# Performance work log

Measured on AMD Instinct MI355X. Metric: run time of the kernel, lower is better.

Reference implementation:

```python
import jax, jax.numpy as jnp
import numpy as np

WIDTH = 64
RANK = 4
CLEVEL = 1
MLEVEL = 2
NB = 4
HID1, HID2 = 64, 128  # DenseNet hidden sizes for phi/psi kernel networks


def setup_inputs() -> dict:
    key = jax.random.key(0)
    ks = jax.random.split(key, 24)
    b, s = 2, 256

    def g(k, shape, fan):
        return jax.random.normal(k, shape, jnp.float32) / np.sqrt(fan)

    L = MLEVEL + 1
    inp = {
        "x": jax.random.normal(ks[0], (b, s, s, 1), jnp.float32),
        "a": jax.random.uniform(ks[1], (b, s, s, 2), jnp.float32),
        # lifting p: Linear(3, width)
        "pW": g(ks[2], (3, WIDTH), 3), "pb": jnp.zeros((WIDTH,), jnp.float32),
        # projection q: DenseNet([width, 2*width, 1], ReLU)
        "q1W": g(ks[3], (WIDTH, 2 * WIDTH), WIDTH), "q1b": jnp.zeros((2 * WIDTH,), jnp.float32),
        "q2W": g(ks[4], (2 * WIDTH, 1), 2 * WIDTH), "q2b": jnp.zeros((1,), jnp.float32),
        # low-rank kernel nets phi/psi: DenseNet([3, 64, 128, width*rank]), one per block (stacked)
        "phiW1": g(ks[5], (NB, 3, HID1), 3), "phib1": jnp.zeros((NB, HID1), jnp.float32),
        "phiW2": g(ks[6], (NB, HID1, HID2), HID1), "phib2": jnp.zeros((NB, HID2), jnp.float32),
        "phiW3": g(ks[7], (NB, HID2, WIDTH * RANK), HID2), "phib3": jnp.zeros((NB, WIDTH * RANK), jnp.float32),
        "psiW1": g(ks[8], (NB, 3, HID1), 3), "psib1": jnp.zeros((NB, HID1), jnp.float32),
        "psiW2": g(ks[9], (NB, HID1, HID2), HID1), "psib2": jnp.zeros((NB, HID2), jnp.float32),
        "psiW3": g(ks[10], (NB, HID2, WIDTH * RANK), HID2), "psib3": jnp.zeros((NB, WIDTH * RANK), jnp.float32),
        # per-block LayerNorm(width)
        "lnG": jnp.ones((NB, WIDTH), jnp.float32), "lnB": jnp.zeros((NB, WIDTH), jnp.float32),
        # per-block multi-level local-correction 3x3 convs (OIHW), levels 0..MLEVEL
        "convW": g(ks[11], (NB, L, WIDTH, WIDTH, 3, 3), WIDTH * 9),
        "convb": jnp.zeros((NB, L, WIDTH), jnp.float32),
    }
    return inp


def _mlp3(x, W1, b1, W2, b2, W3, b3):
    h = jax.nn.relu(x @ W1 + b1)
    h = jax.nn.relu(h @ W2 + b2)
    return h @ W3 + b3


def _lowrank(v, a, phi_p, psi_p):
    # v: (b, sx, sy, w) features; a: (b, sx, sy, 3) coords+input
    b, sx, sy, w = v.shape
    n = sx * sy
    af = a.reshape(b, n, 3)
    vf = v.reshape(b, n, w)
    phi = _mlp3(af, *phi_p).reshape(b, n, w, RANK)  # (b,n,w,r)
    psi = _mlp3(af, *psi_p).reshape(b, n, w, RANK)
    # K(u)(x_m) = sum_r phi_r(x_m) * (1/n) sum_n psi_r(y_n) u(y_n), per channel
    y = jnp.einsum("bnwr,bnw->bwr", psi, vf) / n
    out = jnp.einsum("bnwr,bwr->bnw", phi, y)
    return out.reshape(b, sx, sy, w)


def _conv3x3(x, W, bias):
    # x: (b,c,h,w) NCHW, W: (o,i,3,3)
    y = jax.lax.conv_general_dilated(x, W, (1, 1), "SAME",
                                     dimension_numbers=("NCHW", "OIHW", "NCHW"))
    return y + bias[None, :, None, None]


def _local_correction(xc, Ws, bs):
    # xc: (b,c,h,w); Ws: (L,o,i,3,3); multi-level conv pyramid, bilinear upsample back
    h, w = xc.shape[2], xc.shape[3]
    out = _conv3x3(xc, Ws[0], bs[0])
    for l in range(1, Ws.shape[0]):
        xl = xc[:, :, :: 2 ** l, :: 2 ** l]
        yl = _conv3x3(xl, Ws[l], bs[l])
        out = out + jax.image.resize(yl, yl.shape[:2] + (h, w), method="bilinear")
    return out


def _layernorm(x, g, b, eps=1e-5):
    mu = jnp.mean(x, axis=-1, keepdims=True)
    var = jnp.mean(jnp.square(x - mu), axis=-1, keepdims=True)
    return (x - mu) * jax.lax.rsqrt(var + eps) * g + b


def reference(x, a, pW, pb, q1W, q1b, q2W, q2b,
              phiW1, phib1, phiW2, phib2, phiW3, phib3,
              psiW1, psib1, psiW2, psib2, psiW3, psib3,
              lnG, lnB, convW, convb):
    b, sx, sy, _ = x.shape
    xa = jnp.concatenate([a, x], axis=-1)  # (b,sx,sy,3)
    acat = xa
    h = xa @ pW + pb  # lift to width
    c = 2 ** CLEVEL
    for i in range(NB):
        # local correction branch (NCHW conv pyramid)
        x1 = _local_correction(h.transpose(0, 3, 1, 2), convW[i], convb[i]).transpose(0, 2, 3, 1)
        # low-rank kernel integral on coarsened grid, then bilinear upsample
        hd = h[:, ::c, ::c]
        ad = acat[:, ::c, ::c]
        x2 = _lowrank(hd, ad,
                      (phiW1[i], phib1[i], phiW2[i], phib2[i], phiW3[i], phib3[i]),
                      (psiW1[i], psib1[i], psiW2[i], psib2[i], psiW3[i], psib3[i]))
        x2 = jax.image.resize(x2.transpose(0, 3, 1, 2), (b, WIDTH, sx, sy),
                              method="bilinear").transpose(0, 2, 3, 1)
        h = _layernorm(x1 + x2, lnG[i], lnB[i])
        if i != NB - 1:
            h = jax.nn.relu(h)
    h1 = jax.nn.relu(h @ q1W + q1b)
    return h1 @ q2W + q2b
```

## Files before the change

kernel.cpp:

```cpp
#include <hip/hip_runtime.h>
#include <cstddef>
#include <cstdint>


static constexpr size_t OFF_X1     = 0;
static constexpr size_t OFF_YL1    = 4194304;
static constexpr size_t OFF_YL2    = 5242880;
static constexpr size_t OFF_HBF    = 5505024;
static constexpr size_t OFF_H2PSI  = 9699328;
static constexpr size_t OFF_H2PHI  = 11796480;
static constexpr size_t OFF_CWTBF  = 13893632;
static constexpr size_t OFF_Q1BF   = 14114816;
static constexpr size_t OFF_W2T    = 14118912;
static constexpr size_t OFF_GPART  = 14151680;
static constexpr size_t OFF_SVP    = 18345984;
static constexpr size_t OFF_G      = 18378752;
static constexpr size_t OFF_SV     = 18395136;
static constexpr size_t OFF_C      = 18395264;
static constexpr size_t OFF_D      = 18411648;

typedef __attribute__((ext_vector_type(8)))  short bf16x8_t;
typedef __attribute__((ext_vector_type(16))) float f32x16_t;

__device__ inline float wave_sum64(float v) {
    v += __shfl_xor(v, 1);
    v += __shfl_xor(v, 2);
    v += __shfl_xor(v, 4);
    v += __shfl_xor(v, 8);
    v += __shfl_xor(v, 16);
    v += __shfl_xor(v, 32);
    return v;
}

__device__ inline unsigned short f2bf(float f) {
    uint32_t u = __float_as_uint(f);
    uint32_t r = u + 0x7FFFu + ((u >> 16) & 1u);
    return (unsigned short)(r >> 16);
}
__device__ inline float bf2f(unsigned short u) {
    return __uint_as_float((uint32_t)u << 16);
}
__device__ inline void bf8_to_f(uint4 u, float* d) {
    unsigned uv[4] = {u.x, u.y, u.z, u.w};
#pragma unroll
    for (int i = 0; i < 4; ++i) {
        d[2 * i]     = __uint_as_float((uv[i] & 0xFFFFu) << 16);
        d[2 * i + 1] = __uint_as_float(uv[i] & 0xFFFF0000u);
    }
}

__device__ inline size_t fullpix(int b, int n) {
    return (size_t)(b * 65536 + (n >> 7) * 512 + ((n & 127) << 1));
}

struct Lerp { int i0, i1; float f; };
__device__ inline Lerp lcoord(int o, float r, float off, int Sin) {
    float s = fmaxf(fmaf((float)o, r, off), 0.f);
    Lerp L;
    L.i0 = (int)s;
    L.f  = s - (float)L.i0;
    L.i1 = min(L.i0 + 1, Sin - 1);
    return L;
}

__global__ __launch_bounds__(256) void k_setup(const float* __restrict__ convW,
                                               unsigned short* __restrict__ cwt,
                                               const float* __restrict__ q1W,
                                               unsigned short* __restrict__ q1bf,
                                               const float* __restrict__ psiW2,
                                               const float* __restrict__ phiW2,
                                               unsigned short* __restrict__ w2t,
                                               const float* __restrict__ x,
                                               const float* __restrict__ a,
                                               const float* __restrict__ pW,
                                               const float* __restrict__ pb,
                                               unsigned short* __restrict__ hbf) {
    int bid = blockIdx.x;
    int t = threadIdx.x;
    if (bid < 1728) {
        int idx = bid * 256 + t;
        if (idx >= 442368) return;
        int j    = idx & 7;
        int oc   = (idx >> 3) & 63;
        int hi   = (idx >> 9) & 1;
        int kq   = (idx >> 10) & 3;
        int rest = idx >> 12;
        int tap  = rest % 9;
        int il   = rest / 9;
        int ic   = kq * 16 + hi * 8 + j;
        cwt[idx] = f2bf(convW[((size_t)(il * 64 + oc) * 64 + ic) * 9 + tap]);
    } else if (bid < 1760) {
        int idx = (bid - 1728) * 256 + t;
        int k = idx & 63;
        int j = idx >> 6;
        q1bf[j * 64 + k] = f2bf(q1W[k * 128 + j]);
    } else if (bid < 2016) {
        int idx = (bid - 1760) * 256 + t;
        int jj = idx & 7;
        int lo = (idx >> 3) & 31;
        int hi = (idx >> 8) & 1;
        int kq = (idx >> 9) & 3;
        int jt = (idx >> 11) & 3;
        int i  = (idx >> 13) & 3;
        int m  = idx >> 15;
        int k  = kq * 16 + hi * 8 + jj;
        int j  = jt * 32 + lo;
        const float* W2 = m ? phiW2 : psiW2;
        w2t[idx] = f2bf(W2[(size_t)i * 8192 + k * 128 + j]);
    } else {
        int p = (bid - 2016) * 256 + t;
        float a0 = a[(size_t)p * 2 + 0];
        float a1 = a[(size_t)p * 2 + 1];
        float xv = x[p];
        float vals[64];
#pragma unroll
        for (int c = 0; c < 64; ++c)
            vals[c] = fmaf(a0, pW[c], fmaf(a1, pW[64 + c], fmaf(xv, pW[128 + c], pb[c])));
        unsigned short us[64];
#pragma unroll
        for (int c = 0; c < 64; ++c) us[c] = f2bf(vals[c]);
        unsigned short* bp = hbf + (size_t)p * 64;
#pragma unroll
        for (int c = 0; c < 64; c += 8)
            *(uint4*)(bp + c) = *(uint4*)(us + c);
    }
}

__global__ __launch_bounds__(256) void k_convmlp(
    const unsigned short* __restrict__ hbf,
    const unsigned short* __restrict__ wbf,
    const float* __restrict__ convb,
    unsigned short* __restrict__ x1, unsigned short* __restrict__ yl1,
    unsigned short* __restrict__ yl2,
    const float* __restrict__ a, const float* __restrict__ x,
    const float* __restrict__ W1a, const float* __restrict__ b1a,
    const float* __restrict__ b2a,
    const float* __restrict__ W1b, const float* __restrict__ b1b,
    const float* __restrict__ b2b,
    const unsigned short* __restrict__ w2t,
    unsigned short* __restrict__ H2a, unsigned short* __restrict__ H2b,
    int iter) {
    __shared__ unsigned short Ald[20736];
    int bid = blockIdx.x;
    int t = threadIdx.x;

    if (bid >= 672) {
        int blk = bid - 672;
        int m = blk >> 9;
        int px0 = (blk & 511) << 6;
        const float* W1 = m ? W1b : W1a;
        const float* b1 = m ? b1b : b1a;
        const float* b2 = m ? b2b : b2a;
        unsigned short* H2 = m ? H2b : H2a;

        int w    = t >> 6;
        int lane = t & 63;
        int lo   = lane & 31;
        int hi   = lane >> 5;

        int pxlA = px0 + lo, pxlB = px0 + 32 + lo;
        int bA = pxlA >> 14;
        size_t apA = fullpix(bA, pxlA & 16383);
        size_t apB = fullpix(bA, pxlB & 16383);
        float a0A = a[apA * 2], a1A = a[apA * 2 + 1], xvA = x[apA];
        float a0B = a[apB * 2], a1B = a[apB * 2 + 1], xvB = x[apB];

        bf16x8_t faA[4], faB[4];
#pragma unroll
        for (int kq = 0; kq < 4; ++kq) {
            unsigned short tA[8], tB[8];
#pragma unroll
            for (int jj = 0; jj < 8; ++jj) {
                int k = kq * 16 + hi * 8 + jj;
                float w1a = W1[k], w1b = W1[64 + k], w1c = W1[128 + k], bb = b1[k];
                tA[jj] = f2bf(fmaxf(fmaf(a0A, w1a, fmaf(a1A, w1b, fmaf(xvA, w1c, bb))), 0.f));
                tB[jj] = f2bf(fmaxf(fmaf(a0B, w1a, fmaf(a1B, w1b, fmaf(xvB, w1c, bb))), 0.f));
            }
            faA[kq] = *(bf16x8_t*)tA;
            faB[kq] = *(bf16x8_t*)tB;
        }
        const unsigned short* wb =
            w2t + (size_t)(((m * 4 + iter) * 4 + w) * 4) * 512 + hi * 256 + lo * 8;
        f32x16_t accA = {}, accB = {};
#pragma unroll
        for (int kq = 0; kq < 4; ++kq) {
            bf16x8_t fb = *(const bf16x8_t*)(wb + kq * 512);
            accA = __builtin_amdgcn_mfma_f32_32x32x16_bf16(faA[kq], fb, accA, 0, 0, 0);
            accB = __builtin_amdgcn_mfma_f32_32x32x16_bf16(faB[kq], fb, accB, 0, 0, 0);
        }
        float bias2 = b2[w * 32 + lo];
#pragma unroll
        for (int reg = 0; reg < 16; ++reg) {
            int row = (reg & 3) + 8 * (reg >> 2) + 4 * hi;
            H2[(size_t)(px0 + row) * 128 + w * 32 + lo]      = f2bf(fmaxf(accA[reg] + bias2, 0.f));
            H2[(size_t)(px0 + 32 + row) * 128 + w * 32 + lo] = f2bf(fmaxf(accB[reg] + bias2, 0.f));
        }
        return;
    }

    int lvl, tix, Sl, st, tpr;
    if (bid < 512)      { lvl = 0; tix = bid;       Sl = 256; st = 1; tpr = 16; }
    else if (bid < 640) { lvl = 1; tix = bid - 512; Sl = 128; st = 2; tpr = 8;  }
    else                { lvl = 2; tix = bid - 640; Sl = 64;  st = 4; tpr = 4;  }
    int tpb = tpr * tpr;
    int b = tix / tpb;
    int r = tix - b * tpb;
    int y0 = (r / tpr) * 16, x0 = (r % tpr) * 16;

    for (int c = t; c < 2592; c += 256) {
        int lin = c >> 3, slot = c & 7;
        int ty = lin / 18, tx = lin - ty * 18;
        int oy = y0 + ty - 1, ox = x0 + tx - 1;
        uint4 val = make_uint4(0u, 0u, 0u, 0u);
        if ((unsigned)oy < (unsigned)Sl && (unsigned)ox < (unsigned)Sl) {
            const unsigned short* src =
                hbf + (((size_t)(b * 256 + oy * st) * 256 + ox * st) << 6) + (slot << 3);
            val = *(const uint4*)src;
        }
        int byte = (lin << 7) + (((slot ^ (lin & 7))) << 4);
        *(uint4*)((char*)Ald + byte) = val;
    }
    __syncthreads();

    int w    = t >> 6;
    int lane = t & 63;
    int lo   = lane & 31;
    int hi   = lane >> 5;
    f32x16_t acc00 = {}, acc01 = {}, acc10 = {}, acc11 = {};

    const unsigned short* wbase =
        wbf + (size_t)(iter * 3 + lvl) * 36864 + hi * 512 + lo * 8;

    int yA0 = 4 * w + (lo >> 4);
    int xA  = lo & 15;

    bf16x8_t v0c[4], v1c[4], v0n[4], v1n[4];
#pragma unroll
    for (int kq = 0; kq < 4; ++kq) {
        v0c[kq] = *(const bf16x8_t*)(wbase + kq * 1024);
        v1c[kq] = *(const bf16x8_t*)(wbase + kq * 1024 + 256);
    }
#pragma unroll
    for (int tap = 0; tap < 9; ++tap) {
        if (tap < 8) {
#pragma unroll
            for (int kq = 0; kq < 4; ++kq) {
                int keo = ((tap + 1) * 4 + kq) * 1024;
                v0n[kq] = *(const bf16x8_t*)(wbase + keo);
                v1n[kq] = *(const bf16x8_t*)(wbase + keo + 256);
            }
        }
        int dy = tap / 3, dx = tap - dy * 3;
        int lin0 = (yA0 + dy) * 18 + (xA + dx);
        int lin1 = lin0 + 36;
#pragma unroll
        for (int kq = 0; kq < 4; ++kq) {
            int icb = (kq << 5) + (hi << 4);
            int a0b = ((lin0 << 7) + icb) ^ ((lin0 & 7) << 4);
            int a1b = ((lin1 << 7) + icb) ^ ((lin1 & 7) << 4);
            bf16x8_t va0 = *(bf16x8_t*)((char*)Ald + a0b);
            bf16x8_t va1 = *(bf16x8_t*)((char*)Ald + a1b);
            acc00 = __builtin_amdgcn_mfma_f32_32x32x16_bf16(va0, v0c[kq], acc00, 0, 0, 0);
            acc01 = __builtin_amdgcn_mfma_f32_32x32x16_bf16(va0, v1c[kq], acc01, 0, 0, 0);
            acc10 = __builtin_amdgcn_mfma_f32_32x32x16_bf16(va1, v0c[kq], acc10, 0, 0, 0);
            acc11 = __builtin_amdgcn_mfma_f32_32x32x16_bf16(va1, v1c[kq], acc11, 0, 0, 0);
        }
#pragma unroll
        for (int kq = 0; kq < 4; ++kq) { v0c[kq] = v0n[kq]; v1c[kq] = v1n[kq]; }
    }

    unsigned short* out = (lvl == 0) ? x1 : (lvl == 1 ? yl1 : yl2);
    const float* bias = convb + (iter * 3 + lvl) * 64;
    float bias0 = bias[lo];
    float bias1 = bias[32 + lo];
#pragma unroll
    for (int reg = 0; reg < 16; ++reg) {
        int row = (reg & 3) + 8 * (reg >> 2) + 4 * hi;
        int yt  = 4 * w + (row >> 4);
        int xt  = row & 15;
        size_t pix0 = ((size_t)(b * Sl + y0 + yt) * Sl + (x0 + xt)) << 6;
        out[pix0 + lo]      = f2bf(acc00[reg] + bias0);
        out[pix0 + 32 + lo] = f2bf(acc01[reg] + bias1);
        size_t pix1 = ((size_t)(b * Sl + y0 + yt + 2) * Sl + (x0 + xt)) << 6;
        out[pix1 + lo]      = f2bf(acc10[reg] + bias0);
        out[pix1 + 32 + lo] = f2bf(acc11[reg] + bias1);
    }
}

__global__ __launch_bounds__(256) void k_gpart(const unsigned short* __restrict__ hbf,
                                               const unsigned short* __restrict__ H2psi,
                                               float* __restrict__ Gpart,
                                               float* __restrict__ svpart) {
    __shared__ float vt[4096];
    __shared__ float h2t[8192];
    int blk = blockIdx.x;
    int b = blk >> 8;
    int n0 = (blk & 255) << 6;
    int t = threadIdx.x;
    int pxq = t >> 2, qq = t & 3;
    int sw = (pxq & 7) << 4;
    {
        const unsigned short* src = hbf + fullpix(b, n0 + pxq) * 64 + qq * 16;
        uint4 u0 = *(const uint4*)src;
        uint4 u1 = *(const uint4*)(src + 8);
        float f[16];
        bf8_to_f(u0, f);
        bf8_to_f(u1, f + 8);
#pragma unroll
        for (int j = 0; j < 4; ++j) {
            int byte = (pxq * 256 + qq * 64 + j * 16) ^ sw;
            *(float4*)((char*)vt + byte) = make_float4(f[4 * j], f[4 * j + 1],
                                                       f[4 * j + 2], f[4 * j + 3]);
        }
        const unsigned short* hsrc = H2psi + ((size_t)(b * 16384 + n0 + pxq)) * 128 + qq * 32;
#pragma unroll
        for (int rr = 0; rr < 4; ++rr) {
            uint4 hu = *(const uint4*)(hsrc + rr * 8);
            float g[8];
            bf8_to_f(hu, g);
            int byte0 = (pxq * 512 + qq * 128 + rr * 32) ^ sw;
            int byte1 = (pxq * 512 + qq * 128 + rr * 32 + 16) ^ sw;
            *(float4*)((char*)h2t + byte0) = make_float4(g[0], g[1], g[2], g[3]);
            *(float4*)((char*)h2t + byte1) = make_float4(g[4], g[5], g[6], g[7]);
        }
    }
    __syncthreads();

    int wt_ = (t >> 5) << 3;
    int kt  = (t & 31) << 2;
    float acc[8][4];
#pragma unroll
    for (int i = 0; i < 8; ++i)
#pragma unroll
        for (int j = 0; j < 4; ++j) acc[i][j] = 0.f;

#pragma unroll 4
    for (int nn = 0; nn < 64; ++nn) {
        int nsw = (nn & 7) << 4;
        float4 hv = *(float4*)((char*)h2t + ((nn * 512 + kt * 4) ^ nsw));
        float4 v0 = *(float4*)((char*)vt + ((nn * 256 + wt_ * 4) ^ nsw));
        float4 v1 = *(float4*)((char*)vt + ((nn * 256 + wt_ * 4 + 16) ^ nsw));
        float vv[8] = {v0.x, v0.y, v0.z, v0.w, v1.x, v1.y, v1.z, v1.w};
        float hh[4] = {hv.x, hv.y, hv.z, hv.w};
#pragma unroll
        for (int i = 0; i < 8; ++i)
#pragma unroll
            for (int j = 0; j < 4; ++j) acc[i][j] = fmaf(vv[i], hh[j], acc[i][j]);
    }

    float* gp = Gpart + (size_t)blk * 8192;
#pragma unroll
    for (int i = 0; i < 8; ++i)
        *(float4*)&gp[(wt_ + i) * 128 + kt] =
            make_float4(acc[i][0], acc[i][1], acc[i][2], acc[i][3]);

    if (t < 64) {
        float s = 0.f;
#pragma unroll 8
        for (int p = 0; p < 64; ++p)
            s += *(float*)((char*)vt + ((p * 256 + t * 4) ^ ((p & 7) << 4)));
        svpart[blk * 64 + t] = s;
    }
}

__global__ __launch_bounds__(256) void k_gred(const float* __restrict__ Gpart,
                                              const float* __restrict__ svpart,
                                              float* __restrict__ G,
                                              float* __restrict__ sv) {
    __shared__ float red[4][64];
    int blk = blockIdx.x;
    int t = threadIdx.x;
    if (blk < 256) {
        int b  = blk >> 7;
        int es = (blk & 127) << 6;
        int e  = es + (t & 63);
        int cg = t >> 6;
        float s = 0.f;
        const float* gp = Gpart + ((size_t)(b * 256 + cg * 64)) * 8192 + e;
#pragma unroll 8
        for (int c = 0; c < 64; ++c) s += gp[(size_t)c * 8192];
        red[cg][t & 63] = s;
        __syncthreads();
        if (t < 64)
            G[b * 8192 + es + t] = red[0][t] + red[1][t] + red[2][t] + red[3][t];
    } else {
        int b = blk - 256;
        int w = t & 63, cg = t >> 6;
        float s = 0.f;
        const float* sp = svpart + ((size_t)(b * 256 + cg * 64)) * 64 + w;
#pragma unroll 8
        for (int c = 0; c < 64; ++c) s += sp[c * 64];
        red[cg][w] = s;
        __syncthreads();
        if (t < 64) sv[b * 64 + t] = red[0][t] + red[1][t] + red[2][t] + red[3][t];
    }
}

__global__ __launch_bounds__(256) void k_yc(const float* __restrict__ G,
                                            const float* __restrict__ sv,
                                            const float* __restrict__ W3psi,
                                            const float* __restrict__ b3psi,
                                            const float* __restrict__ W3phi,
                                            const float* __restrict__ b3phi,
                                            float* __restrict__ C,
                                            float* __restrict__ D) {
    __shared__ float ybar[256];
    int bq = blockIdx.x;
    int b = bq >> 4, q = bq & 15;
    int t = threadIdx.x;
    {
        int o = t, w = o >> 2;
        const float* gp = &G[(size_t)(b * 64 + w) * 128];
        float s0 = 0.f, s1 = 0.f, s2 = 0.f, s3 = 0.f;
#pragma unroll 4
        for (int k = 0; k < 128; k += 4) {
            s0 = fmaf(W3psi[(k + 0) * 256 + o], gp[k + 0], s0);
            s1 = fmaf(W3psi[(k + 1) * 256 + o], gp[k + 1], s1);
            s2 = fmaf(W3psi[(k + 2) * 256 + o], gp[k + 2], s2);
            s3 = fmaf(W3psi[(k + 3) * 256 + o], gp[k + 3], s3);
        }
        float s = b3psi[o] * sv[b * 64 + w] + ((s0 + s1) + (s2 + s3));
        ybar[o] = s * (1.f / 16384.f);
    }
    __syncthreads();
#pragma unroll
    for (int rep = 0; rep < 2; ++rep) {
        int e = q * 512 + rep * 256 + t;
        int w = e >> 7, k = e & 127;
        const float* wp = &W3phi[k * 256 + w * 4];
        C[b * 8192 + e] = fmaf(wp[0], ybar[w * 4],
                          fmaf(wp[1], ybar[w * 4 + 1],
                          fmaf(wp[2], ybar[w * 4 + 2], wp[3] * ybar[w * 4 + 3])));
    }
    if (q == 0 && t < 64) {
        int w = t;
        D[b * 64 + w] = b3phi[w * 4] * ybar[w * 4] + b3phi[w * 4 + 1] * ybar[w * 4 + 1]
                      + b3phi[w * 4 + 2] * ybar[w * 4 + 2] + b3phi[w * 4 + 3] * ybar[w * 4 + 3];
    }
}

__global__ __launch_bounds__(256) void k_x2c(const unsigned short* __restrict__ H2phi,
                                             const float* __restrict__ C,
                                             const float* __restrict__ D,
                                             unsigned short* __restrict__ x2c) {
    __shared__ float cl[8192];
    __shared__ float h2l[4096];
    __shared__ float Dl[64];
    int blk = blockIdx.x;
    int b = blk >> 9;
    int px0 = (blk & 511) << 5;
    int t = threadIdx.x;

    const float* cp = C + b * 8192;
#pragma unroll
    for (int r = 0; r < 8; ++r) {
        int f = r * 1024 + t * 4;
        *(float4*)&cl[f] = *(const float4*)&cp[f];
    }
    if (t < 64) Dl[t] = D[b * 64 + t];
    {
        const unsigned short* hsrc = H2phi + ((size_t)(b * 16384 + px0)) * 128;
#pragma unroll
        for (int r = 0; r < 2; ++r) {
            int f = r * 2048 + t * 8;
            uint4 u = *(const uint4*)(hsrc + f);
            float d[8];
            bf8_to_f(u, d);
            int px = f >> 7;
            int sw2 = ((px & 7) << 4) ^ (((px >> 3) & 1) << 6);
            *(float4*)((char*)h2l + ((f * 4) ^ sw2))      = make_float4(d[0], d[1], d[2], d[3]);
            *(float4*)((char*)h2l + ((f * 4 + 16) ^ sw2)) = make_float4(d[4], d[5], d[6], d[7]);
        }
    }
    __syncthreads();

    int px = t & 31;
    int w0 = (t >> 5) << 3;
    int psw = ((px & 7) << 4) ^ (((px >> 3) & 1) << 6);
    float acc[8];
#pragma unroll
    for (int j = 0; j < 8; ++j) acc[j] = 0.f;

#pragma unroll 4
    for (int kq = 0; kq < 32; ++kq) {
        float4 hq = *(float4*)((char*)h2l + ((px * 512 + kq * 16) ^ psw));
#pragma unroll
        for (int j = 0; j < 8; ++j) {
            float4 cq = *(float4*)&cl[(w0 + j) * 128 + kq * 4];
            acc[j] = fmaf(hq.x, cq.x, acc[j]);
            acc[j] = fmaf(hq.y, cq.y, acc[j]);
            acc[j] = fmaf(hq.z, cq.z, acc[j]);
            acc[j] = fmaf(hq.w, cq.w, acc[j]);
        }
    }
    unsigned short us[8];
#pragma unroll
    for (int j = 0; j < 8; ++j) us[j] = f2bf(acc[j] + Dl[w0 + j]);
    unsigned short* op = x2c + ((size_t)(b * 16384 + px0 + px)) * 64 + w0;
    *(uint4*)op = *(uint4*)us;
}

__global__ __launch_bounds__(256) void k_epilogue(const unsigned short* __restrict__ x1,
                                                  const unsigned short* __restrict__ yl1,
                                                  const unsigned short* __restrict__ yl2,
                                                  const unsigned short* __restrict__ x2c,
                                                  const float* __restrict__ lnG,
                                                  const float* __restrict__ lnB,
                                                  unsigned short* __restrict__ hbf,
                                                  int do_relu) {
    __shared__ float y1s[2][10][64];
    __shared__ float xcs[2][10][64];
    __shared__ float y2s[2][6][64];
    int t    = threadIdx.x;
    int blk  = blockIdx.x;
    int b    = blk >> 12;
    int rest = blk & 4095;
    int y    = rest >> 4;
    int x0   = (rest & 15) << 4;
    int wv = t >> 6, lane = t & 63;

    Lerp ly1 = lcoord(y, 0.5f, -0.25f, 128);
    Lerp ly2 = lcoord(y, 0.25f, -0.375f, 64);
    int c1 = max(0, (int)floorf((float)x0 * 0.5f - 0.25f));
    int c2 = max(0, (int)floorf((float)x0 * 0.25f - 0.375f));

    const unsigned short* Y1 = yl1 + (size_t)b * 16384 * 64;
    const unsigned short* Y2 = yl2 + (size_t)b * 4096 * 64;
    const unsigned short* XC = x2c + (size_t)b * 16384 * 64;
    for (int f4 = t; f4 < 832; f4 += 256) {
        int e, row, col;
        const unsigned short* src;
        float* dst;
        if (f4 < 320) {
            e = f4 * 4;
            int r = e / 640, rm = e - r * 640;
            int j = rm >> 6, ch = rm & 63;
            row = r ? ly1.i1 : ly1.i0;
            col = min(c1 + j, 127);
            src = &Y1[((size_t)(row * 128 + col)) * 64 + ch];
            dst = &y1s[r][j][ch];
        } else if (f4 < 640) {
            e = (f4 - 320) * 4;
            int r = e / 640, rm = e - r * 640;
            int j = rm >> 6, ch = rm & 63;
            row = r ? ly1.i1 : ly1.i0;
            col = min(c1 + j, 127);
            src = &XC[((size_t)(row * 128 + col)) * 64 + ch];
            dst = &xcs[r][j][ch];
        } else {
            e = (f4 - 640) * 4;
            int r = e / 384, rm = e - r * 384;
            int j = rm >> 6, ch = rm & 63;
            row = r ? ly2.i1 : ly2.i0;
            col = min(c2 + j, 63);
            src = &Y2[((size_t)(row * 64 + col)) * 64 + ch];
            dst = &y2s[r][j][ch];
        }
        uint2 u = *(const uint2*)src;
        dst[0] = __uint_as_float((u.x & 0xFFFFu) << 16);
        dst[1] = __uint_as_float(u.x & 0xFFFF0000u);
        dst[2] = __uint_as_float((u.y & 0xFFFFu) << 16);
        dst[3] = __uint_as_float(u.y & 0xFFFF0000u);
    }
    __syncthreads();

    float g = lnG[lane], be = lnB[lane];
    for (int pp = 0; pp < 4; ++pp) {
        int xx = x0 + wv * 4 + pp;
        size_t pix = (size_t)((b * 256 + y) * 256 + xx);
        float v = bf2f(x1[pix * 64 + lane]);
        {
            Lerp lx = lcoord(xx, 0.5f, -0.25f, 128);
            int j0 = lx.i0 - c1, j1 = lx.i1 - c1;
            float a0 = y1s[0][j0][lane], a1 = y1s[0][j1][lane];
            float b0 = y1s[1][j0][lane], b1 = y1s[1][j1][lane];
            float ta = a0 + lx.f * (a1 - a0);
            float tb = b0 + lx.f * (b1 - b0);
            v += ta + ly1.f * (tb - ta);
            float p0 = xcs[0][j0][lane], p1 = xcs[0][j1][lane];
            float q0 = xcs[1][j0][lane], q1 = xcs[1][j1][lane];
            float tp = p0 + lx.f * (p1 - p0);
            float tq = q0 + lx.f * (q1 - q0);
            v += tp + ly1.f * (tq - tp);
        }
        {
            Lerp lx = lcoord(xx, 0.25f, -0.375f, 64);
            int j0 = lx.i0 - c2, j1 = lx.i1 - c2;
            float a0 = y2s[0][j0][lane], a1 = y2s[0][j1][lane];
            float b0 = y2s[1][j0][lane], b1 = y2s[1][j1][lane];
            float ta = a0 + lx.f * (a1 - a0);
            float tb = b0 + lx.f * (b1 - b0);
            v += ta + ly2.f * (tb - ta);
        }
        float mu  = wave_sum64(v) * (1.f / 64.f);
        float d   = v - mu;
        float var = wave_sum64(d * d) * (1.f / 64.f);
        float ov  = fmaf(d * rsqrtf(var + 1e-5f), g, be);
        if (do_relu) ov = fmaxf(ov, 0.f);
        hbf[pix * 64 + lane] = f2bf(ov);
    }
}

__global__ __launch_bounds__(256) void k_head_mfma(
    const unsigned short* __restrict__ hbf,
    const unsigned short* __restrict__ q1bf,
    const float* __restrict__ q1b,
    const float* __restrict__ q2,
    const float* __restrict__ q2b,
    float* __restrict__ out) {
    __shared__ unsigned short Q[8192];
    int t = threadIdx.x;
    for (int c = t; c < 1024; c += 256) {
        int j = c >> 3, slot = c & 7;
        uint4 v = *(const uint4*)(q1bf + j * 64 + slot * 8);
        int byte = (j * 128 + slot * 16) ^ ((j & 7) << 4);
        *(uint4*)((char*)Q + byte) = v;
    }
    __syncthreads();

    int w = t >> 6, lane = t & 63;
    int lo = lane & 31, hi = lane >> 5;
    int px0 = blockIdx.x * 128 + w * 32;

    bf16x8_t av[4];
    const unsigned short* hp = hbf + (size_t)(px0 + lo) * 64 + hi * 8;
#pragma unroll
    for (int ks = 0; ks < 4; ++ks)
        av[ks] = *(const bf16x8_t*)(hp + ks * 16);

    float res[16];
#pragma unroll
    for (int r = 0; r < 16; ++r) res[r] = 0.f;

#pragma unroll
    for (int jb = 0; jb < 4; ++jb) {
        f32x16_t acc = {};
        int j = jb * 32 + lo;
#pragma unroll
        for (int ks = 0; ks < 4; ++ks) {
            int byte = (j * 128 + ks * 32 + hi * 16) ^ ((j & 7) << 4);
            bf16x8_t bv = *(bf16x8_t*)((char*)Q + byte);
            acc = __builtin_amdgcn_mfma_f32_32x32x16_bf16(av[ks], bv, acc, 0, 0, 0);
        }
        float b1 = q1b[j];
        float w2 = q2[j];
#pragma unroll
        for (int r = 0; r < 16; ++r)
            res[r] = fmaf(fmaxf(acc[r] + b1, 0.f), w2, res[r]);
    }
#pragma unroll
    for (int r = 0; r < 16; ++r) {
        float v = res[r];
        v += __shfl_xor(v, 1);
        v += __shfl_xor(v, 2);
        v += __shfl_xor(v, 4);
        v += __shfl_xor(v, 8);
        v += __shfl_xor(v, 16);
        res[r] = v;
    }
    if (lo == 0) {
        float qb = q2b[0];
#pragma unroll
        for (int r = 0; r < 16; ++r) {
            int row = (r & 3) + 8 * (r >> 2) + 4 * hi;
            out[px0 + row] = res[r] + qb;
        }
    }
}

extern "C" void kernel_launch(void* const* d_in, const int* in_sizes, int n_in,
                              void* d_out, int out_size, void* d_ws, size_t ws_size,
                              hipStream_t stream) {
    const float* x     = (const float*)d_in[0];
    const float* a     = (const float*)d_in[1];
    const float* pW    = (const float*)d_in[2];
    const float* pb    = (const float*)d_in[3];
    const float* q1W   = (const float*)d_in[4];
    const float* q1b   = (const float*)d_in[5];
    const float* q2W   = (const float*)d_in[6];
    const float* q2b   = (const float*)d_in[7];
    const float* phiW1 = (const float*)d_in[8];
    const float* phib1 = (const float*)d_in[9];
    const float* phiW2 = (const float*)d_in[10];
    const float* phib2 = (const float*)d_in[11];
    const float* phiW3 = (const float*)d_in[12];
    const float* phib3 = (const float*)d_in[13];
    const float* psiW1 = (const float*)d_in[14];
    const float* psib1 = (const float*)d_in[15];
    const float* psiW2 = (const float*)d_in[16];
    const float* psib2 = (const float*)d_in[17];
    const float* psiW3 = (const float*)d_in[18];
    const float* psib3 = (const float*)d_in[19];
    const float* lnG   = (const float*)d_in[20];
    const float* lnB   = (const float*)d_in[21];
    const float* convW = (const float*)d_in[22];
    const float* convb = (const float*)d_in[23];

    float* ws = (float*)d_ws;
    unsigned short* x1    = (unsigned short*)(ws + OFF_X1);
    unsigned short* yl1   = (unsigned short*)(ws + OFF_YL1);
    unsigned short* yl2   = (unsigned short*)(ws + OFF_YL2);
    unsigned short* hbf   = (unsigned short*)(ws + OFF_HBF);
    unsigned short* H2psi = (unsigned short*)(ws + OFF_H2PSI);
    unsigned short* x2c   = (unsigned short*)(ws + OFF_H2PSI);
    unsigned short* H2phi = (unsigned short*)(ws + OFF_H2PHI);
    unsigned short* cwtbf = (unsigned short*)(ws + OFF_CWTBF);
    unsigned short* q1bf  = (unsigned short*)(ws + OFF_Q1BF);
    unsigned short* w2t   = (unsigned short*)(ws + OFF_W2T);
    float* Gpart = ws + OFF_GPART;
    float* svpart= ws + OFF_SVP;
    float* G     = ws + OFF_G;
    float* sv    = ws + OFF_SV;
    float* C     = ws + OFF_C;
    float* D     = ws + OFF_D;

    k_setup<<<2528, 256, 0, stream>>>(convW, cwtbf, q1W, q1bf,
                                      psiW2, phiW2, w2t, x, a, pW, pb, hbf);

    for (int i = 0; i < 4; ++i) {
        k_convmlp<<<1696, 256, 0, stream>>>(hbf, cwtbf, convb, x1, yl1, yl2,
                                            a, x,
                                            psiW1 + i * 192, psib1 + i * 64, psib2 + i * 128,
                                            phiW1 + i * 192, phib1 + i * 64, phib2 + i * 128,
                                            w2t, H2psi, H2phi, i);
        k_gpart<<<512, 256, 0, stream>>>(hbf, H2psi, Gpart, svpart);
        k_gred<<<258, 256, 0, stream>>>(Gpart, svpart, G, sv);
        k_yc<<<32, 256, 0, stream>>>(G, sv,
                                     psiW3 + (size_t)i * 32768, psib3 + i * 256,
                                     phiW3 + (size_t)i * 32768, phib3 + i * 256,
                                     C, D);
        k_x2c<<<1024, 256, 0, stream>>>(H2phi, C, D, x2c);
        k_epilogue<<<8192, 256, 0, stream>>>(x1, yl1, yl2, x2c,
                                             lnG + i * 64, lnB + i * 64,
                                             hbf, (i < 3) ? 1 : 0);
    }

    k_head_mfma<<<1024, 256, 0, stream>>>(hbf, q1bf, q1b, q2W, q2b, (float*)d_out);
}
```

Before: 426.1 us.

## Fuse yc into x2c kernel and stage conv outputs through LDS for coalesced stores

Merges the small k_yc kernel into k_x2c. Each of the 1024 blocks now recomputes ybar, the C matrix and D directly into shared memory, which removes one launch per block iteration and the global round trip for C and D. The cost is redundant work: every block redoes the W3psi/W3phi matvecs and reads 32K floats of W3phi. Separately, the conv kernel now writes its MFMA accumulators into the LDS A-tile buffer and then issues 16-byte coalesced global stores, replacing the scattered 2-byte stores.

Result: slower. 469.1 us (+10.1%).

```diff
diff --git a/kernel.cpp b/kernel.cpp
--- a/kernel.cpp
+++ b/kernel.cpp
@@ -16,8 +16,6 @@
 static constexpr size_t OFF_SVP    = 18345984;
 static constexpr size_t OFF_G      = 18378752;
 static constexpr size_t OFF_SV     = 18395136;
-static constexpr size_t OFF_C      = 18395264;
-static constexpr size_t OFF_D      = 18411648;
 
 typedef __attribute__((ext_vector_type(8)))  short bf16x8_t;
 typedef __attribute__((ext_vector_type(16))) float f32x16_t;
@@ -269,7 +267,8 @@
         for (int kq = 0; kq < 4; ++kq) { v0c[kq] = v0n[kq]; v1c[kq] = v1n[kq]; }
     }
 
-    unsigned short* out = (lvl == 0) ? x1 : (lvl == 1 ? yl1 : yl2);
+    __syncthreads();
+    unsigned short* Cld = Ald;
     const float* bias = convb + (iter * 3 + lvl) * 64;
     float bias0 = bias[lo];
     float bias1 = bias[32 + lo];
@@ -278,12 +277,22 @@
         int row = (reg & 3) + 8 * (reg >> 2) + 4 * hi;
         int yt  = 4 * w + (row >> 4);
         int xt  = row & 15;
-        size_t pix0 = ((size_t)(b * Sl + y0 + yt) * Sl + (x0 + xt)) << 6;
-        out[pix0 + lo]      = f2bf(acc00[reg] + bias0);
-        out[pix0 + 32 + lo] = f2bf(acc01[reg] + bias1);
-        size_t pix1 = ((size_t)(b * Sl + y0 + yt + 2) * Sl + (x0 + xt)) << 6;
-        out[pix1 + lo]      = f2bf(acc10[reg] + bias0);
-        out[pix1 + 32 + lo] = f2bf(acc11[reg] + bias1);
+        int px0l = (yt * 16 + xt) << 6;
+        Cld[px0l + lo]      = f2bf(acc00[reg] + bias0);
+        Cld[px0l + 32 + lo] = f2bf(acc01[reg] + bias1);
+        int px1l = ((yt + 2) * 16 + xt) << 6;
+        Cld[px1l + lo]      = f2bf(acc10[reg] + bias0);
+        Cld[px1l + 32 + lo] = f2bf(acc11[reg] + bias1);
+    }
+    __syncthreads();
+    unsigned short* out = (lvl == 0) ? x1 : (lvl == 1 ? yl1 : yl2);
+#pragma unroll
+    for (int rr = 0; rr < 8; ++rr) {
+        int f  = rr * 256 + t;
+        int yt = f >> 7;
+        int c  = f & 127;
+        unsigned short* dst = out + (((size_t)(b * Sl + y0 + yt) * Sl + x0) << 6) + c * 8;
+        *(uint4*)dst = ((const uint4*)Cld)[f];
     }
 }
 
@@ -396,18 +405,37 @@
     }
 }
 
-__global__ __launch_bounds__(256) void k_yc(const float* __restrict__ G,
-                                            const float* __restrict__ sv,
-                                            const float* __restrict__ W3psi,
-                                            const float* __restrict__ b3psi,
-                                            const float* __restrict__ W3phi,
-                                            const float* __restrict__ b3phi,
-                                            float* __restrict__ C,
-                                            float* __restrict__ D) {
+__global__ __launch_bounds__(256) void k_x2cyc(const float* __restrict__ G,
+                                               const float* __restrict__ sv,
+                                               const float* __restrict__ W3psi,
+                                               const float* __restrict__ b3psi,
+                                               const float* __restrict__ W3phi,
+                                               const float* __restrict__ b3phi,
+                                               const unsigned short* __restrict__ H2phi,
+                                               unsigned short* __restrict__ x2c) {
     __shared__ float ybar[256];
-    int bq = blockIdx.x;
-    int b = bq >> 4, q = bq & 15;
+    __shared__ float cl[8192];
+    __shared__ float h2l[4096];
+    __shared__ float Dl[64];
+    int blk = blockIdx.x;
+    int b = blk >> 9;
+    int px0 = (blk & 511) << 5;
     int t = threadIdx.x;
+
+    {
+        const unsigned short* hsrc = H2phi + ((size_t)(b * 16384 + px0)) * 128;
+#pragma unroll
+        for (int r = 0; r < 2; ++r) {
+            int f = r * 2048 + t * 8;
+            uint4 u = *(const uint4*)(hsrc + f);
+            float d[8];
+            bf8_to_f(u, d);
+            int px = f >> 7;
+            int sw2 = ((px & 7) << 4) ^ (((px >> 3) & 1) << 6);
+            *(float4*)((char*)h2l + ((f * 4) ^ sw2))      = make_float4(d[0], d[1], d[2], d[3]);
+            *(float4*)((char*)h2l + ((f * 4 + 16) ^ sw2)) = make_float4(d[4], d[5], d[6], d[7]);
+        }
+    }
     {
         int o = t, w = o >> 2;
         const float* gp = &G[(size_t)(b * 64 + w) * 128];
@@ -424,53 +452,17 @@
     }
     __syncthreads();
 #pragma unroll
-    for (int rep = 0; rep < 2; ++rep) {
-        int e = q * 512 + rep * 256 + t;
+    for (int rep = 0; rep < 32; ++rep) {
+        int e = rep * 256 + t;
         int w = e >> 7, k = e & 127;
         const float* wp = &W3phi[k * 256 + w * 4];
-        C[b * 8192 + e] = fmaf(wp[0], ybar[w * 4],
-                          fmaf(wp[1], ybar[w * 4 + 1],
-                          fmaf(wp[2], ybar[w * 4 + 2], wp[3] * ybar[w * 4 + 3])));
-    }
-    if (q == 0 && t < 64) {
-        int w = t;
-        D[b * 64 + w] = b3phi[w * 4] * ybar[w * 4] + b3phi[w * 4 + 1] * ybar[w * 4 + 1]
-                      + b3phi[w * 4 + 2] * ybar[w * 4 + 2] + b3phi[w * 4 + 3] * ybar[w * 4 + 3];
-    }
-}
-
-__global__ __launch_bounds__(256) void k_x2c(const unsigned short* __restrict__ H2phi,
-                                             const float* __restrict__ C,
-                                             const float* __restrict__ D,
-                                             unsigned short* __restrict__ x2c) {
-    __shared__ float cl[8192];
-    __shared__ float h2l[4096];
-    __shared__ float Dl[64];
-    int blk = blockIdx.x;
-    int b = blk >> 9;
-    int px0 = (blk & 511) << 5;
-    int t = threadIdx.x;
-
-    const float* cp = C + b * 8192;
-#pragma unroll
-    for (int r = 0; r < 8; ++r) {
-        int f = r * 1024 + t * 4;
-        *(float4*)&cl[f] = *(const float4*)&cp[f];
-    }
-    if (t < 64) Dl[t] = D[b * 64 + t];
-    {
-        const unsigned short* hsrc = H2phi + ((size_t)(b * 16384 + px0)) * 128;
-#pragma unroll
-        for (int r = 0; r < 2; ++r) {
-            int f = r * 2048 + t * 8;
-            uint4 u = *(const uint4*)(hsrc + f);
-            float d[8];
-            bf8_to_f(u, d);
-            int px = f >> 7;
-            int sw2 = ((px & 7) << 4) ^ (((px >> 3) & 1) << 6);
-            *(float4*)((char*)h2l + ((f * 4) ^ sw2))      = make_float4(d[0], d[1], d[2], d[3]);
-            *(float4*)((char*)h2l + ((f * 4 + 16) ^ sw2)) = make_float4(d[4], d[5], d[6], d[7]);
-        }
+        cl[e] = fmaf(wp[0], ybar[w * 4],
+                fmaf(wp[1], ybar[w * 4 + 1],
+                fmaf(wp[2], ybar[w * 4 + 2], wp[3] * ybar[w * 4 + 3])));
+    }
+    if (t < 64) {
+        Dl[t] = b3phi[t * 4] * ybar[t * 4] + b3phi[t * 4 + 1] * ybar[t * 4 + 1]
+              + b3phi[t * 4 + 2] * ybar[t * 4 + 2] + b3phi[t * 4 + 3] * ybar[t * 4 + 3];
     }
     __syncthreads();
 
@@ -711,8 +703,6 @@
     float* svpart= ws + OFF_SVP;
     float* G     = ws + OFF_G;
     float* sv    = ws + OFF_SV;
-    float* C     = ws + OFF_C;
-    float* D     = ws + OFF_D;
 
     k_setup<<<2528, 256, 0, stream>>>(convW, cwtbf, q1W, q1bf,
                                       psiW2, phiW2, w2t, x, a, pW, pb, hbf);
@@ -725,11 +715,10 @@
                                             w2t, H2psi, H2phi, i);
         k_gpart<<<512, 256, 0, stream>>>(hbf, H2psi, Gpart, svpart);
         k_gred<<<258, 256, 0, stream>>>(Gpart, svpart, G, sv);
-        k_yc<<<32, 256, 0, stream>>>(G, sv,
-                                     psiW3 + (size_t)i * 32768, psib3 + i * 256,
-                                     phiW3 + (size_t)i * 32768, phib3 + i * 256,
-                                     C, D);
-        k_x2c<<<1024, 256, 0, stream>>>(H2phi, C, D, x2c);
+        k_x2cyc<<<1024, 256, 0, stream>>>(G, sv,
+                                          psiW3 + (size_t)i * 32768, psib3 + i * 256,
+                                          phiW3 + (size_t)i * 32768, phib3 + i * 256,
+                                          H2phi, x2c);
         k_epilogue<<<8192, 256, 0, stream>>>(x1, yl1, yl2, x2c,
                                              lnG + i * 64, lnB + i * 64,
                                              hbf, (i < 3) ? 1 : 0);
```
